# Kernel tuning notes

Hardware: AMD Instinct MI355X
Metric: run time of the kernel (lower is better)

The kernel has to match this reference:

```python
import jax, jax.numpy as jnp
import numpy as np

W_PRIMAL, W_DUAL, W_STAT, W_COMP = 0.1, 0.1, 0.6, 0.2

B_ = 64
M_PER = 2048
N_PER = 2048
E = 8388608
SUM_M = B_ * M_PER
SUM_N = B_ * N_PER


def setup_inputs() -> dict:
    key = jax.random.key(0)
    k1, k2, k3, k4, k5, k6, k7 = jax.random.split(key, 7)
    return {
        "x_hat": jax.random.normal(k1, (SUM_N,), dtype=jnp.float32),
        "lam_hat": jax.random.normal(k2, (SUM_M,), dtype=jnp.float32),
        "edge_rows": jax.random.randint(k3, (E,), 0, SUM_M, dtype=jnp.int32),
        "edge_cols": jax.random.randint(k4, (E,), 0, SUM_N, dtype=jnp.int32),
        "edge_attr": jax.random.normal(k5, (E,), dtype=jnp.float32),
        "b_pad": jax.random.normal(k6, (B_, M_PER), dtype=jnp.float32),
        "c_pad": jax.random.normal(k7, (B_, N_PER), dtype=jnp.float32),
        "B": B_,
        "m_per": M_PER,
        "n_per": N_PER,
    }


def reference(x_hat, lam_hat, edge_rows, edge_cols, edge_attr, b_pad, c_pad, B, m_per, n_per):
    sum_m = B * m_per
    sum_n = B * n_per
    # masks are all-True (uniform instance sizes) -> b_pad[b_mask] == flatten
    b_cat = b_pad.reshape(-1).astype(jnp.float32)  # [sum_m]
    c_cat = c_pad.reshape(-1).astype(jnp.float32)  # [sum_n]

    x = x_hat.astype(jnp.float32)
    l = lam_hat.astype(jnp.float32)
    a = edge_attr.astype(jnp.float32)

    # SpMV via edge-list scatter-add: Ax and A^T lam
    Ax = jnp.zeros(sum_m, jnp.float32).at[edge_rows].add(a * x[edge_cols])
    ATlam = jnp.zeros(sum_n, jnp.float32).at[edge_cols].add(a * l[edge_rows])

    Ax_minus_b = Ax - b_cat
    primal_vec = jax.nn.relu(Ax_minus_b)
    dual_vec = jax.nn.relu(-l)
    stat_vec = ATlam + c_cat
    compl_vec = l * Ax_minus_b

    row_batch = jnp.repeat(jnp.arange(B, dtype=jnp.int32), m_per)  # [sum_m]
    col_batch = jnp.repeat(jnp.arange(B, dtype=jnp.int32), n_per)  # [sum_n]

    def seg_mean_sq(vec, seg, count):
        sums = jax.ops.segment_sum(vec * vec, seg, num_segments=B)
        return sums / jnp.float32(max(count, 1))

    loss_pr = seg_mean_sq(primal_vec, row_batch, m_per).sum()
    loss_du = seg_mean_sq(dual_vec, row_batch, m_per).sum()
    loss_st = seg_mean_sq(stat_vec, col_batch, n_per).sum()
    loss_cs = seg_mean_sq(compl_vec, row_batch, m_per).sum()

    total = (W_PRIMAL * loss_pr + W_DUAL * loss_du
             + W_STAT * loss_st + W_COMP * loss_cs) / jnp.float32(B)
    return total
```

## Files before the change

kernel.cpp:

```cpp
#include <hip/hip_runtime.h>
#include <stdint.h>

static constexpr int THREADS = 256;
static constexpr int SCAN_THREADS = 1024;
static constexpr int LOSS_BLOCKS = 512;
static constexpr int CM  = 16384;
static constexpr int CN  = 16384;
static constexpr int CSZ = CM + CN;
static constexpr int REP_T = 32;
static constexpr int MAX_REP = 32;

typedef int   vint4   __attribute__((ext_vector_type(4)));
typedef float vfloat4 __attribute__((ext_vector_type(4)));

template <int REP>
__global__ __launch_bounds__(SCAN_THREADS) void kkt_scan_t(
    const int* __restrict__ rows, const int* __restrict__ cols,
    const float* __restrict__ attr,
    const float* __restrict__ x, const float* __restrict__ lam,
    float* __restrict__ partial, int E) {
  __shared__ float lds[CSZ];
  const int p = blockIdx.x / REP;
  const int r = blockIdx.x % REP;
  const unsigned baseM = (unsigned)(p * CM);
  const unsigned baseN = (unsigned)(p * CN);

  vfloat4* l4 = (vfloat4*)lds;
  for (int i = threadIdx.x; i < CSZ / 4; i += SCAN_THREADS) l4[i] = (vfloat4)(0.0f);
  __syncthreads();

  long per = (((long)E + REP - 1) / REP + 3) & ~3L;
  long e0 = per * r;  if (e0 > E) e0 = E;
  long e1 = e0 + per; if (e1 > E) e1 = E;
  long n4 = (e1 - e0) >> 2;

  const vint4*   rows4 = (const vint4*)(rows + e0);
  const vint4*   cols4 = (const vint4*)(cols + e0);
  const vfloat4* attr4 = (const vfloat4*)(attr + e0);
  const int tid = threadIdx.x;

  for (long q = tid; q < n4; q += SCAN_THREADS) {
    vint4   rr = rows4[q];
    vint4   cc = cols4[q];
    vfloat4 aa = attr4[q];
#define EDGE_ACC(RR, CC, AA)                                                 \
    do {                                                                     \
      unsigned mm = (unsigned)(RR) - baseM;                                  \
      if (mm < (unsigned)CM) unsafeAtomicAdd(&lds[mm], (AA) * x[(CC)]);      \
      unsigned nn = (unsigned)(CC) - baseN;                                  \
      if (nn < (unsigned)CN) unsafeAtomicAdd(&lds[CM + nn], (AA) * lam[(RR)]); \
    } while (0)
    EDGE_ACC(rr.x, cc.x, aa.x);
    EDGE_ACC(rr.y, cc.y, aa.y);
    EDGE_ACC(rr.z, cc.z, aa.z);
    EDGE_ACC(rr.w, cc.w, aa.w);
  }
  for (long i = e0 + (n4 << 2) + tid; i < e1; i += SCAN_THREADS) {
    int rv = rows[i], cv = cols[i];
    float a = attr[i];
    EDGE_ACC(rv, cv, a);
  }
#undef EDGE_ACC

  __syncthreads();
  vfloat4* d4 = (vfloat4*)(partial + (size_t)(p * REP + r) * CSZ);
  for (int i = threadIdx.x; i < CSZ / 4; i += SCAN_THREADS)
    __builtin_nontemporal_store(l4[i], d4 + i);
}

template <int REP>
__global__ __launch_bounds__(THREADS) void kkt_loss_t(
    const float* __restrict__ partial,
    const float* __restrict__ bcat, const float* __restrict__ ccat,
    const float* __restrict__ lam, double* __restrict__ bacc,
    int sum_m, int sum_n) {
  long idx = (long)blockIdx.x * THREADS + threadIdx.x;
  long stride = (long)gridDim.x * THREADS;
  long total = (long)sum_m + sum_n;
  double pr = 0.0, du = 0.0, st = 0.0, cs = 0.0;
  for (long i = idx; i < total; i += stride) {
    if (i < sum_m) {
      int ii = (int)i;
      int p = ii / CM, j = ii % CM;
      const float* b = partial + (size_t)(p * REP) * CSZ + j;
      float ax = 0.0f;
#pragma unroll
      for (int s = 0; s < REP; ++s)
        ax += __builtin_nontemporal_load(b + (size_t)s * CSZ);
      float d  = ax - bcat[ii];
      float li = lam[ii];
      float pp   = d > 0.0f ? d : 0.0f;
      float u    = li < 0.0f ? -li : 0.0f;
      float comp = li * d;
      pr += (double)pp * pp;
      du += (double)u * u;
      cs += (double)comp * comp;
    } else {
      int ii = (int)(i - sum_m);
      int p = ii / CN, j = ii % CN;
      const float* b = partial + (size_t)(p * REP) * CSZ + CM + j;
      float at = 0.0f;
#pragma unroll
      for (int s = 0; s < REP; ++s)
        at += __builtin_nontemporal_load(b + (size_t)s * CSZ);
      float sv = at + ccat[ii];
      st += (double)sv * sv;
    }
  }
  for (int off = 32; off > 0; off >>= 1) {
    pr += __shfl_down(pr, off);
    du += __shfl_down(du, off);
    st += __shfl_down(st, off);
    cs += __shfl_down(cs, off);
  }
  __shared__ double sred[THREADS / 64][4];
  const int wv = threadIdx.x >> 6;
  if ((threadIdx.x & 63) == 0) {
    sred[wv][0] = pr; sred[wv][1] = du; sred[wv][2] = st; sred[wv][3] = cs;
  }
  __syncthreads();
  if (threadIdx.x == 0) {
    double a0 = 0, a1 = 0, a2 = 0, a3 = 0;
#pragma unroll
    for (int w = 0; w < THREADS / 64; ++w) {
      a0 += sred[w][0]; a1 += sred[w][1]; a2 += sred[w][2]; a3 += sred[w][3];
    }
    bacc[(size_t)blockIdx.x * 4 + 0] = a0;
    bacc[(size_t)blockIdx.x * 4 + 1] = a1;
    bacc[(size_t)blockIdx.x * 4 + 2] = a2;
    bacc[(size_t)blockIdx.x * 4 + 3] = a3;
  }
}

__global__ __launch_bounds__(THREADS) void kkt_finalize_fast(
    const double* __restrict__ bacc, int nblk,
    const int* __restrict__ Bp, const int* __restrict__ mp,
    const int* __restrict__ np_, float* __restrict__ out) {
  double v0 = 0, v1 = 0, v2 = 0, v3 = 0;
  for (int i = threadIdx.x; i < nblk; i += THREADS) {
    v0 += bacc[(size_t)i * 4 + 0];
    v1 += bacc[(size_t)i * 4 + 1];
    v2 += bacc[(size_t)i * 4 + 2];
    v3 += bacc[(size_t)i * 4 + 3];
  }
  for (int off = 32; off > 0; off >>= 1) {
    v0 += __shfl_down(v0, off);
    v1 += __shfl_down(v1, off);
    v2 += __shfl_down(v2, off);
    v3 += __shfl_down(v3, off);
  }
  __shared__ double sred[THREADS / 64][4];
  const int wv = threadIdx.x >> 6;
  if ((threadIdx.x & 63) == 0) {
    sred[wv][0] = v0; sred[wv][1] = v1; sred[wv][2] = v2; sred[wv][3] = v3;
  }
  __syncthreads();
  if (threadIdx.x == 0) {
    double a0 = 0, a1 = 0, a2 = 0, a3 = 0;
#pragma unroll
    for (int w = 0; w < THREADS / 64; ++w) {
      a0 += sred[w][0]; a1 += sred[w][1]; a2 += sred[w][2]; a3 += sred[w][3];
    }
    double m = (double)mp[0];
    double n = (double)np_[0];
    double B = (double)Bp[0];
    out[0] = (float)((0.1 * (a0 + a1) / m + 0.6 * a2 / n + 0.2 * a3 / m) / B);
  }
}

__global__ void kkt_init(double* __restrict__ acc, float* __restrict__ out) {
  int t = threadIdx.x;
  if (t < 4) acc[t] = 0.0;
  if (t == 0) out[0] = 0.0f;
}

__global__ __launch_bounds__(SCAN_THREADS) void kkt_scan_dyn(
    const int* __restrict__ rows, const int* __restrict__ cols,
    const float* __restrict__ attr,
    const float* __restrict__ x, const float* __restrict__ lam,
    float* __restrict__ partial, int E, int REP) {
  __shared__ float lds[CSZ];
  const int p = blockIdx.x / REP;
  const int r = blockIdx.x % REP;
  const int baseM = p * CM;
  const int baseN = p * CN;
  vfloat4* l4 = (vfloat4*)lds;
  for (int i = threadIdx.x; i < CSZ / 4; i += SCAN_THREADS) l4[i] = (vfloat4)(0.0f);
  __syncthreads();
  long per = (((long)E + REP - 1) / REP + 3) & ~3L;
  long e0 = per * r;  if (e0 > E) e0 = E;
  long e1 = e0 + per; if (e1 > E) e1 = E;
  int  n4 = (int)((e1 - e0) >> 2);
  const vint4*   rows4 = (const vint4*)(rows + e0);
  const vint4*   cols4 = (const vint4*)(cols + e0);
  const vfloat4* attr4 = (const vfloat4*)(attr + e0);
#define EDGE_ACC(RR, CC, AA)                                                 \
  do {                                                                       \
    unsigned mm = (unsigned)((RR) - baseM);                                  \
    if (mm < (unsigned)CM) unsafeAtomicAdd(&lds[mm], (AA) * x[(CC)]);        \
    unsigned nn = (unsigned)((CC) - baseN);                                  \
    if (nn < (unsigned)CN) unsafeAtomicAdd(&lds[CM + nn], (AA) * lam[(RR)]); \
  } while (0)
  for (int i = threadIdx.x; i < n4; i += SCAN_THREADS) {
    vint4 rr = rows4[i]; vint4 cc = cols4[i]; vfloat4 aa = attr4[i];
    EDGE_ACC(rr.x, cc.x, aa.x);
    EDGE_ACC(rr.y, cc.y, aa.y);
    EDGE_ACC(rr.z, cc.z, aa.z);
    EDGE_ACC(rr.w, cc.w, aa.w);
  }
  for (long i = e0 + ((long)n4 << 2) + threadIdx.x; i < e1; i += SCAN_THREADS) {
    int rr = rows[i], cc = cols[i];
    float aa = attr[i];
    EDGE_ACC(rr, cc, aa);
  }
#undef EDGE_ACC
  __syncthreads();
  vfloat4* d4 = (vfloat4*)(partial + (size_t)(p * REP + r) * CSZ);
  for (int i = threadIdx.x; i < CSZ / 4; i += SCAN_THREADS) d4[i] = l4[i];
}

__global__ __launch_bounds__(THREADS) void kkt_loss_dyn(
    const float* __restrict__ partial,
    const float* __restrict__ bcat, const float* __restrict__ ccat,
    const float* __restrict__ lam, double* __restrict__ acc,
    int sum_m, int sum_n, int REP) {
  int idx = blockIdx.x * blockDim.x + threadIdx.x;
  int stride = gridDim.x * blockDim.x;
  double pr = 0.0, du = 0.0, st = 0.0, cs = 0.0;
  for (int i = idx; i < sum_m; i += stride) {
    int p = i / CM, j = i - p * CM;
    const float* base = partial + (size_t)(p * REP) * CSZ + j;
    float ax = 0.0f;
    for (int rr = 0; rr < REP; ++rr) ax += base[(size_t)rr * CSZ];
    float d  = ax - bcat[i];
    float li = lam[i];
    float pp   = d > 0.0f ? d : 0.0f;
    float u    = li < 0.0f ? -li : 0.0f;
    float comp = li * d;
    pr += (double)pp * pp;
    du += (double)u * u;
    cs += (double)comp * comp;
  }
  for (int i = idx; i < sum_n; i += stride) {
    int p = i / CN, j = i - p * CN;
    const float* base = partial + (size_t)(p * REP) * CSZ + CM + j;
    float at = 0.0f;
    for (int rr = 0; rr < REP; ++rr) at += base[(size_t)rr * CSZ];
    float s = at + ccat[i];
    st += (double)s * s;
  }
  for (int off = 32; off > 0; off >>= 1) {
    pr += __shfl_down(pr, off);
    du += __shfl_down(du, off);
    st += __shfl_down(st, off);
    cs += __shfl_down(cs, off);
  }
  if ((threadIdx.x & 63) == 0) {
    unsafeAtomicAdd(&acc[0], pr);
    unsafeAtomicAdd(&acc[1], du);
    unsafeAtomicAdd(&acc[2], st);
    unsafeAtomicAdd(&acc[3], cs);
  }
}

__global__ void kkt_finalize(const double* __restrict__ acc,
                             const int* __restrict__ Bp,
                             const int* __restrict__ mp,
                             const int* __restrict__ np_,
                             float* __restrict__ out) {
  double m = (double)mp[0];
  double n = (double)np_[0];
  double B = (double)Bp[0];
  double total =
      (0.1 * (acc[0] + acc[1]) / m + 0.6 * acc[2] / n + 0.2 * acc[3] / m) / B;
  out[0] = (float)total;
}

extern "C" void kernel_launch(void* const* d_in, const int* in_sizes, int n_in,
                              void* d_out, int out_size, void* d_ws, size_t ws_size,
                              hipStream_t stream) {
  const float* x    = (const float*)d_in[0];
  const float* lam  = (const float*)d_in[1];
  const int*   rows = (const int*)d_in[2];
  const int*   cols = (const int*)d_in[3];
  const float* attr = (const float*)d_in[4];
  const float* bcat = (const float*)d_in[5];
  const float* ccat = (const float*)d_in[6];
  const int*   Bp   = (const int*)d_in[7];
  const int*   mp   = (const int*)d_in[8];
  const int*   np_  = (const int*)d_in[9];

  const int sum_n = in_sizes[0];
  const int sum_m = in_sizes[1];
  const int E     = in_sizes[2];

  char*   ws   = (char*)d_ws;
  double* acc  = (double*)ws;
  double* bacc = (double*)(ws + 256);
  float*  buf  = (float*)(ws + 256 + LOSS_BLOCKS * 4 * sizeof(double));
  float*  out  = (float*)d_out;

  const int NPm = (sum_m + CM - 1) / CM;
  const int NPn = (sum_n + CN - 1) / CN;
  const int NP  = NPm > NPn ? NPm : NPn;

  const size_t head = 256 + (size_t)LOSS_BLOCKS * 4 * sizeof(double);
  size_t avail = ws_size > head ? ws_size - head : 0;
  const size_t need_t = (size_t)NP * REP_T * CSZ * sizeof(float);

  if (avail >= need_t) {
    kkt_scan_t<REP_T><<<NP * REP_T, SCAN_THREADS, 0, stream>>>(
        rows, cols, attr, x, lam, buf, E);
    kkt_loss_t<REP_T><<<LOSS_BLOCKS, THREADS, 0, stream>>>(
        buf, bcat, ccat, lam, bacc, sum_m, sum_n);
    kkt_finalize_fast<<<1, THREADS, 0, stream>>>(bacc, LOSS_BLOCKS, Bp, mp,
                                                 np_, out);
  } else {
    float* fbuf = (float*)(ws + 64);
    size_t favail = ws_size > 64 ? ws_size - 64 : 0;
    int REP = (int)(favail / ((size_t)NP * CSZ * sizeof(float)));
    if (REP > MAX_REP) REP = MAX_REP;
    if (REP < 1) REP = 1;
    kkt_init<<<1, 64, 0, stream>>>(acc, out);
    kkt_scan_dyn<<<NP * REP, SCAN_THREADS, 0, stream>>>(rows, cols, attr, x,
                                                        lam, fbuf, E, REP);
    int lw = sum_m > sum_n ? sum_m : sum_n;
    int lb = (lw + THREADS - 1) / THREADS;
    if (lb > 1024) lb = 1024;
    kkt_loss_dyn<<<lb, THREADS, 0, stream>>>(fbuf, bcat, ccat, lam, acc,
                                             sum_m, sum_n, REP);
    kkt_finalize<<<1, 1, 0, stream>>>(acc, Bp, mp, np_, out);
  }
}
```

Measured before the change: 136.1 us.

## Split scan blocks into row-side and column-side with larger LDS chunks

Each scan block now accumulates either Ax rows or A^T lam columns over a 32K-entry chunk, instead of both halves with 16K each. This halves the gathers and LDS atomics each block performs per edge while keeping the same grid size and LDS footprint. The partial-buffer layout and the loss kernel indexing are changed to match. Edge-stream traffic stays the same, so the benefit depends on whether the scan is bound by gathers and atomics rather than bandwidth.

```diff
diff --git a/kernel.cpp b/kernel.cpp
--- a/kernel.cpp
+++ b/kernel.cpp
@@ -4,29 +4,31 @@
 static constexpr int THREADS = 256;
 static constexpr int SCAN_THREADS = 1024;
 static constexpr int LOSS_BLOCKS = 512;
+static constexpr int CHUNK = 32768;
+static constexpr int REP_T = 32;
+
 static constexpr int CM  = 16384;
 static constexpr int CN  = 16384;
 static constexpr int CSZ = CM + CN;
-static constexpr int REP_T = 32;
 static constexpr int MAX_REP = 32;
 
 typedef int   vint4   __attribute__((ext_vector_type(4)));
 typedef float vfloat4 __attribute__((ext_vector_type(4)));
 
 template <int REP>
-__global__ __launch_bounds__(SCAN_THREADS) void kkt_scan_t(
+__global__ __launch_bounds__(SCAN_THREADS) void kkt_scan2_t(
     const int* __restrict__ rows, const int* __restrict__ cols,
     const float* __restrict__ attr,
     const float* __restrict__ x, const float* __restrict__ lam,
-    float* __restrict__ partial, int E) {
-  __shared__ float lds[CSZ];
-  const int p = blockIdx.x / REP;
+    float* __restrict__ partial, int E, int NPr) {
+  __shared__ float lds[CHUNK];
+  const int q = blockIdx.x / REP;
   const int r = blockIdx.x % REP;
-  const unsigned baseM = (unsigned)(p * CM);
-  const unsigned baseN = (unsigned)(p * CN);
+  const bool rowside = q < NPr;
+  const unsigned base = (unsigned)((rowside ? q : q - NPr) * CHUNK);
 
   vfloat4* l4 = (vfloat4*)lds;
-  for (int i = threadIdx.x; i < CSZ / 4; i += SCAN_THREADS) l4[i] = (vfloat4)(0.0f);
+  for (int i = threadIdx.x; i < CHUNK / 4; i += SCAN_THREADS) l4[i] = (vfloat4)(0.0f);
   __syncthreads();
 
   long per = (((long)E + REP - 1) / REP + 3) & ~3L;
@@ -39,54 +41,76 @@
   const vfloat4* attr4 = (const vfloat4*)(attr + e0);
   const int tid = threadIdx.x;
 
-  for (long q = tid; q < n4; q += SCAN_THREADS) {
-    vint4   rr = rows4[q];
-    vint4   cc = cols4[q];
-    vfloat4 aa = attr4[q];
-#define EDGE_ACC(RR, CC, AA)                                                 \
-    do {                                                                     \
-      unsigned mm = (unsigned)(RR) - baseM;                                  \
-      if (mm < (unsigned)CM) unsafeAtomicAdd(&lds[mm], (AA) * x[(CC)]);      \
-      unsigned nn = (unsigned)(CC) - baseN;                                  \
-      if (nn < (unsigned)CN) unsafeAtomicAdd(&lds[CM + nn], (AA) * lam[(RR)]); \
-    } while (0)
-    EDGE_ACC(rr.x, cc.x, aa.x);
-    EDGE_ACC(rr.y, cc.y, aa.y);
-    EDGE_ACC(rr.z, cc.z, aa.z);
-    EDGE_ACC(rr.w, cc.w, aa.w);
-  }
-  for (long i = e0 + (n4 << 2) + tid; i < e1; i += SCAN_THREADS) {
-    int rv = rows[i], cv = cols[i];
-    float a = attr[i];
-    EDGE_ACC(rv, cv, a);
-  }
-#undef EDGE_ACC
-
-  __syncthreads();
-  vfloat4* d4 = (vfloat4*)(partial + (size_t)(p * REP + r) * CSZ);
-  for (int i = threadIdx.x; i < CSZ / 4; i += SCAN_THREADS)
+  if (rowside) {
+    for (long qq = tid; qq < n4; qq += SCAN_THREADS) {
+      vint4   rr = rows4[qq];
+      vint4   cc = cols4[qq];
+      vfloat4 aa = attr4[qq];
+#define ROW_ACC(RR, CC, AA)                                                  \
+      do {                                                                   \
+        unsigned k = (unsigned)(RR) - base;                                  \
+        if (k < (unsigned)CHUNK) unsafeAtomicAdd(&lds[k], (AA) * x[(CC)]);   \
+      } while (0)
+      ROW_ACC(rr.x, cc.x, aa.x);
+      ROW_ACC(rr.y, cc.y, aa.y);
+      ROW_ACC(rr.z, cc.z, aa.z);
+      ROW_ACC(rr.w, cc.w, aa.w);
+    }
+    for (long i = e0 + (n4 << 2) + tid; i < e1; i += SCAN_THREADS) {
+      int rv = rows[i], cv = cols[i];
+      float a = attr[i];
+      ROW_ACC(rv, cv, a);
+    }
+#undef ROW_ACC
+  } else {
+    for (long qq = tid; qq < n4; qq += SCAN_THREADS) {
+      vint4   rr = rows4[qq];
+      vint4   cc = cols4[qq];
+      vfloat4 aa = attr4[qq];
+#define COL_ACC(RR, CC, AA)                                                  \
+      do {                                                                   \
+        unsigned k = (unsigned)(CC) - base;                                  \
+        if (k < (unsigned)CHUNK) unsafeAtomicAdd(&lds[k], (AA) * lam[(RR)]); \
+      } while (0)
+      COL_ACC(rr.x, cc.x, aa.x);
+      COL_ACC(rr.y, cc.y, aa.y);
+      COL_ACC(rr.z, cc.z, aa.z);
+      COL_ACC(rr.w, cc.w, aa.w);
+    }
+    for (long i = e0 + (n4 << 2) + tid; i < e1; i += SCAN_THREADS) {
+      int rv = rows[i], cv = cols[i];
+      float a = attr[i];
+      COL_ACC(rv, cv, a);
+    }
+#undef COL_ACC
+  }
+
+  __syncthreads();
+  vfloat4* d4 = (vfloat4*)(partial + (size_t)blockIdx.x * CHUNK);
+  for (int i = threadIdx.x; i < CHUNK / 4; i += SCAN_THREADS)
     __builtin_nontemporal_store(l4[i], d4 + i);
 }
 
 template <int REP>
-__global__ __launch_bounds__(THREADS) void kkt_loss_t(
+__global__ __launch_bounds__(THREADS) void kkt_loss2_t(
     const float* __restrict__ partial,
     const float* __restrict__ bcat, const float* __restrict__ ccat,
     const float* __restrict__ lam, double* __restrict__ bacc,
-    int sum_m, int sum_n) {
+    int sum_m, int sum_n, int NPr) {
   long idx = (long)blockIdx.x * THREADS + threadIdx.x;
   long stride = (long)gridDim.x * THREADS;
   long total = (long)sum_m + sum_n;
+  const size_t col_off = (size_t)NPr * REP * CHUNK;
   double pr = 0.0, du = 0.0, st = 0.0, cs = 0.0;
   for (long i = idx; i < total; i += stride) {
     if (i < sum_m) {
       int ii = (int)i;
-      int p = ii / CM, j = ii % CM;
-      const float* b = partial + (size_t)(p * REP) * CSZ + j;
+      int p = ii / CHUNK, j = ii & (CHUNK - 1);
+      const float* b = partial + (size_t)(p * REP) * CHUNK + j;
       float ax = 0.0f;
 #pragma unroll
       for (int s = 0; s < REP; ++s)
-        ax += __builtin_nontemporal_load(b + (size_t)s * CSZ);
+        ax += __builtin_nontemporal_load(b + (size_t)s * CHUNK);
       float d  = ax - bcat[ii];
       float li = lam[ii];
       float pp   = d > 0.0f ? d : 0.0f;
@@ -97,12 +121,12 @@
       cs += (double)comp * comp;
     } else {
       int ii = (int)(i - sum_m);
-      int p = ii / CN, j = ii % CN;
-      const float* b = partial + (size_t)(p * REP) * CSZ + CM + j;
+      int p = ii / CHUNK, j = ii & (CHUNK - 1);
+      const float* b = partial + col_off + (size_t)(p * REP) * CHUNK + j;
       float at = 0.0f;
 #pragma unroll
       for (int s = 0; s < REP; ++s)
-        at += __builtin_nontemporal_load(b + (size_t)s * CSZ);
+        at += __builtin_nontemporal_load(b + (size_t)s * CHUNK);
       float sv = at + ccat[ii];
       st += (double)sv * sv;
     }
@@ -300,23 +324,26 @@
   float*  buf  = (float*)(ws + 256 + LOSS_BLOCKS * 4 * sizeof(double));
   float*  out  = (float*)d_out;
 
-  const int NPm = (sum_m + CM - 1) / CM;
-  const int NPn = (sum_n + CN - 1) / CN;
-  const int NP  = NPm > NPn ? NPm : NPn;
+  const int NPr = (sum_m + CHUNK - 1) / CHUNK;
+  const int NPc = (sum_n + CHUNK - 1) / CHUNK;
+  const int NQ  = NPr + NPc;
 
   const size_t head = 256 + (size_t)LOSS_BLOCKS * 4 * sizeof(double);
   size_t avail = ws_size > head ? ws_size - head : 0;
-  const size_t need_t = (size_t)NP * REP_T * CSZ * sizeof(float);
+  const size_t need_t = (size_t)NQ * REP_T * CHUNK * sizeof(float);
 
   if (avail >= need_t) {
-    kkt_scan_t<REP_T><<<NP * REP_T, SCAN_THREADS, 0, stream>>>(
-        rows, cols, attr, x, lam, buf, E);
-    kkt_loss_t<REP_T><<<LOSS_BLOCKS, THREADS, 0, stream>>>(
-        buf, bcat, ccat, lam, bacc, sum_m, sum_n);
+    kkt_scan2_t<REP_T><<<NQ * REP_T, SCAN_THREADS, 0, stream>>>(
+        rows, cols, attr, x, lam, buf, E, NPr);
+    kkt_loss2_t<REP_T><<<LOSS_BLOCKS, THREADS, 0, stream>>>(
+        buf, bcat, ccat, lam, bacc, sum_m, sum_n, NPr);
     kkt_finalize_fast<<<1, THREADS, 0, stream>>>(bacc, LOSS_BLOCKS, Bp, mp,
                                                  np_, out);
   } else {
     float* fbuf = (float*)(ws + 64);
+    const int NPm = (sum_m + CM - 1) / CM;
+    const int NPn = (sum_n + CN - 1) / CN;
+    const int NP  = NPm > NPn ? NPm : NPn;
     size_t favail = ws_size > 64 ? ws_size - 64 : 0;
     int REP = (int)(favail / ((size_t)NP * CSZ * sizeof(float)));
     if (REP > MAX_REP) REP = MAX_REP;
```

New measurement: 121.4 us (median of 2 runs). -10.8%, faster.
